# Performance work log

Measured on AMD Instinct MI355X. Metric: run time of the kernel, lower is better.

## Reference

```python
import jax, jax.numpy as jnp
import numpy as np

HID, NH = 2048, 16
QLR, KVLR = 1536, 512
DR, DN, DQK, DV = 64, 128, 192, 128
S = 2048
EPS = 1e-06


def rmsnorm(x, w, eps=EPS):
    return x * jax.lax.rsqrt(jnp.mean(x * x, axis=-1, keepdims=True) + eps) * w


def rope_interleave(x, cos, sin):
    # x: [B,H,S,D]; cos/sin: [B,S,D] (unsqueezed to head dim 1)
    b, h, s, d = x.shape
    # DeepSeek-V3 interleave: (d//2, 2) -> transpose -> flatten
    x = x.reshape(b, h, s, d // 2, 2).swapaxes(3, 4).reshape(b, h, s, d)
    c = cos[:, None, :, :]
    sn = sin[:, None, :, :]
    x1, x2 = x[..., : d // 2], x[..., d // 2:]
    rot = jnp.concatenate([-x2, x1], axis=-1)
    return x * c + rot * sn


def setup_inputs() -> dict:
    key = jax.random.key(0)
    ks = jax.random.split(key, 8)
    hidden_states = jax.random.normal(ks[0], (1, S, HID), dtype=jnp.float32)
    # real RoPE tables for the 64-dim rope part
    inv_freq = 1.0 / (10000.0 ** (np.arange(0, DR, 2, dtype=np.float32) / DR))
    pos = np.arange(S, dtype=np.float32)
    freqs = pos[:, None] * inv_freq[None, :]          # [S, DR/2]
    emb = np.concatenate([freqs, freqs], axis=-1)     # [S, DR]
    cos = jnp.asarray(np.cos(emb), dtype=jnp.float32)[None]
    sin = jnp.asarray(np.sin(emb), dtype=jnp.float32)[None]
    w = 0.02
    wq_a = jax.random.normal(ks[1], (QLR, HID), dtype=jnp.float32) * w
    q_a_ln_w = jnp.ones((QLR,), dtype=jnp.float32)
    wq_b = jax.random.normal(ks[2], (NH * DQK, QLR), dtype=jnp.float32) * w
    wkv_a = jax.random.normal(ks[3], (KVLR + DR, HID), dtype=jnp.float32) * w
    kv_a_ln_w = jnp.ones((KVLR,), dtype=jnp.float32)
    wkv_b = jax.random.normal(ks[4], (NH * (DN + DV), KVLR), dtype=jnp.float32) * w
    wo = jax.random.normal(ks[5], (HID, NH * DV), dtype=jnp.float32) * w
    cu_seqlens = jnp.array([0, S // 2, S], dtype=jnp.int32)  # two packed docs
    return {"hidden_states": hidden_states, "cos": cos, "sin": sin,
            "wq_a": wq_a, "q_a_ln_w": q_a_ln_w, "wq_b": wq_b,
            "wkv_a": wkv_a, "kv_a_ln_w": kv_a_ln_w, "wkv_b": wkv_b,
            "wo": wo, "cu_seqlens": cu_seqlens, "max_seqlen": S // 2}


def reference(hidden_states, cos, sin, wq_a, q_a_ln_w, wq_b, wkv_a, kv_a_ln_w,
              wkv_b, wo, cu_seqlens, max_seqlen):
    B, s, _ = hidden_states.shape
    # LoRA-compressed Q: q_a -> RMSNorm -> q_b
    q = rmsnorm(hidden_states @ wq_a.T, q_a_ln_w) @ wq_b.T       # [B,S,NH*DQK]
    q = q.reshape(B, s, NH, DQK).transpose(0, 2, 1, 3)           # [B,NH,S,DQK]
    q_pass, q_rot = q[..., :DN], q[..., DN:]
    # compressed KV with MQA rope part
    ckv = hidden_states @ wkv_a.T                                 # [B,S,KVLR+DR]
    kv_c, k_rot = ckv[..., :KVLR], ckv[..., KVLR:]
    kv = rmsnorm(kv_c, kv_a_ln_w) @ wkv_b.T                       # [B,S,NH*(DN+DV)]
    kv = kv.reshape(B, s, NH, DN + DV).transpose(0, 2, 1, 3)      # [B,NH,S,DN+DV]
    k_pass, v = kv[..., :DN], kv[..., DN:]
    k_rot = k_rot[:, None, :, :]                                  # [B,1,S,DR]
    q_rot = rope_interleave(q_rot, cos, sin)
    k_rot = rope_interleave(k_rot, cos, sin)
    k_rot = jnp.broadcast_to(k_rot, (B, NH, s, DR))
    qf = jnp.concatenate([q_pass, q_rot], axis=-1)                # [B,NH,S,DQK]
    kf = jnp.concatenate([k_pass, k_rot], axis=-1)                # [B,NH,S,DQK]
    # varlen causal attention: block-diagonal per document + causal
    pos = jnp.arange(s)
    seg = jnp.searchsorted(cu_seqlens[1:], pos, side='right')
    mask = (seg[:, None] == seg[None, :]) & (pos[:, None] >= pos[None, :])
    scale = DQK ** -0.5  # flash default: 1/sqrt(q head dim) (v padded to DQK)
    scores = jnp.einsum('bhqd,bhkd->bhqk', qf, kf) * scale
    scores = jnp.where(mask[None, None], scores, jnp.finfo(scores.dtype).min)
    attn = jax.nn.softmax(scores, axis=-1)
    out = jnp.einsum('bhqk,bhkd->bhqd', attn, v)                  # [B,NH,S,DV]
    out = out.transpose(0, 2, 1, 3).reshape(B, s, NH * DV)
    return out @ wo.T
```

## Files before the change

### kernel.cpp

```cpp
#include <hip/hip_runtime.h>

typedef unsigned short u16;
typedef __attribute__((ext_vector_type(8))) short bf16x8;
typedef __attribute__((ext_vector_type(4))) float f32x4;

#define HID 2048
#define NH 16
#define QLR 1536
#define KVLR 512
#define DR 64
#define DN 128
#define DQK 192
#define DV 128
#define SEQ 2048
#define NKVA 2176
#define SCALE 0.07216878364870323f
#define SCL2 0.1041164359699839f
#define THR2 11.541560327111707f

static __device__ __forceinline__ u16 f2bf(float f) {
  unsigned v = __builtin_bit_cast(unsigned, f);
  v = v + 0x7fffu + ((v >> 16) & 1u);
  return (u16)(v >> 16);
}
static __device__ __forceinline__ float bf2f(u16 u) {
  unsigned v = ((unsigned)u) << 16;
  return __builtin_bit_cast(float, v);
}

#define GLOAD16(gp, lp)                                                        \
  __builtin_amdgcn_global_load_lds(                                            \
      (const __attribute__((address_space(1))) void*)(gp),                     \
      (__attribute__((address_space(3))) void*)(lp), 16, 0, 0)

__global__ void k_convert_all(const float* __restrict__ hs, const float* __restrict__ wq_a,
                              const float* __restrict__ wkv_a, const float* __restrict__ wqb,
                              const float* __restrict__ wkvb, const float* __restrict__ wo,
                              u16* __restrict__ hs_bf, u16* __restrict__ wqkva,
                              u16* __restrict__ wqb_bf, u16* __restrict__ wkvb_bf,
                              u16* __restrict__ wo_bf) {
  const long NQ = 4915200;
  long q = (long)blockIdx.x * blockDim.x + threadIdx.x;
  const long stride = (long)gridDim.x * blockDim.x;
  for (; q < NQ; q += stride) {
    const float* src;
    u16* dst;
    long li;
    bool zero = false;
    if (q < 1048576)        { src = hs;   dst = hs_bf;                      li = q; }
    else if (q < 1835008)   { src = wq_a; dst = wqkva;                      li = q - 1048576; }
    else if (q < 2162688)   { li = q - 1835008; src = wkv_a; dst = wqkva + (size_t)QLR * HID;
                              zero = (li >= 294912); }
    else if (q < 3342336)   { src = wqb;  dst = wqb_bf;                     li = q - 2162688; }
    else if (q < 3866624)   { src = wkvb; dst = wkvb_bf;                    li = q - 3342336; }
    else                    { src = wo;   dst = wo_bf;                      li = q - 3866624; }
    u16 o0 = 0, o1 = 0, o2 = 0, o3 = 0;
    if (!zero) {
      const float4 f = *(const float4*)(src + li * 4);
      o0 = f2bf(f.x); o1 = f2bf(f.y); o2 = f2bf(f.z); o3 = f2bf(f.w);
    }
    u16* d = dst + li * 4;
    d[0] = o0; d[1] = o1; d[2] = o2; d[3] = o3;
  }
}

__global__ void k_rmsnorm2(const float* __restrict__ qkva, const float* __restrict__ qw,
                           const float* __restrict__ kvw, u16* __restrict__ q_ln,
                           u16* __restrict__ kv_ln) {
  const int row = blockIdx.x;
  const int which = blockIdx.y;
  const int t = threadIdx.x;
  const int cols = which ? KVLR : QLR;
  const float inv_cols = which ? (1.0f / KVLR) : (1.0f / QLR);
  const float* x = qkva + (size_t)row * NKVA + (which ? QLR : 0);
  const float* w = which ? kvw : qw;
  u16* Y = (which ? kv_ln : q_ln) + (size_t)row * cols;
  float ss = 0.f;
  for (int i = t * 4; i < cols; i += 1024) {
    float4 v = *(const float4*)(x + i);
    ss += v.x * v.x + v.y * v.y + v.z * v.z + v.w * v.w;
  }
#pragma unroll
  for (int m = 1; m < 64; m <<= 1) ss += __shfl_xor(ss, m, 64);
  __shared__ float red[4];
  if ((t & 63) == 0) red[t >> 6] = ss;
  __syncthreads();
  float tot = red[0] + red[1] + red[2] + red[3];
  float r = rsqrtf(tot * inv_cols + 1e-6f);
  for (int i = t * 4; i < cols; i += 1024) {
    float4 v = *(const float4*)(x + i);
    float4 g = *(const float4*)(w + i);
    u16* y = Y + i;
    y[0] = f2bf(v.x * r * g.x);
    y[1] = f2bf(v.y * r * g.y);
    y[2] = f2bf(v.z * r * g.z);
    y[3] = f2bf(v.w * r * g.w);
  }
}

template <int WN, int NBUF, int MODE>
__global__ __launch_bounds__(512) void k_gemm_nt8(
    const u16* __restrict__ A, const u16* __restrict__ B, void* __restrict__ Cout,
    int M, int N, int K, const float* __restrict__ cosb, const float* __restrict__ sinb,
    u16* __restrict__ out_a, u16* __restrict__ out_b) {
  constexpr int BN = WN * 64;
  constexpr int NST = 2 + WN;
  __shared__ __align__(16) u16 As[NBUF][128 * 64];
  __shared__ __align__(16) u16 Bs[NBUF][BN * 64];
  __shared__ __align__(16) u16 vts[MODE == 3 ? 128 * 130 : 2];
  const int t = threadIdx.x;
  const int lane = t & 63;
  const int w = t >> 6, wr = w >> 2, wc = w & 3;
  const int lm = lane & 15, lg = lane >> 4;

  const int nwg = gridDim.x * gridDim.y;
  int bid = blockIdx.y * gridDim.x + blockIdx.x;
  if ((nwg & 7) == 0) bid = (bid & 7) * (nwg >> 3) + (bid >> 3);
  const int bm = bid % gridDim.y;
  const int bn = bid / gridDim.y;

  const u16* aT = A + (size_t)bm * 128 * K;
  const u16* bT = B + (size_t)bn * BN * K;

#define STAGE8(buf, kt_)                                                       \
  do {                                                                         \
    _Pragma("unroll") for (int i = 0; i < 2; ++i) {                            \
      const int g = t + i * 512, row = g >> 3, slot = (g & 7) ^ (row & 7);     \
      GLOAD16(aT + (size_t)row * K + slot * 8 + (kt_), (u16*)As[buf] + g * 8); \
    }                                                                          \
    _Pragma("unroll") for (int i = 0; i < WN; ++i) {                           \
      const int g = t + i * 512, row = g >> 3, slot = (g & 7) ^ (row & 7);     \
      GLOAD16(bT + (size_t)row * K + slot * 8 + (kt_), (u16*)Bs[buf] + g * 8); \
    }                                                                          \
  } while (0)

  f32x4 acc[4][WN] = {};
  const int nk = K >> 6;
#pragma unroll
  for (int b = 0; b < NBUF; ++b)
    if (b < nk) STAGE8(b, b << 6);
  int bt = 0;
  for (int kt = 0; kt < nk; ++kt) {
    const int rem = nk - 1 - kt;
    if constexpr (NBUF == 3) {
      if (rem >= 2)      asm volatile("s_waitcnt vmcnt(%0)" :: "i"(2 * NST) : "memory");
      else if (rem == 1) asm volatile("s_waitcnt vmcnt(%0)" :: "i"(NST) : "memory");
      else               asm volatile("s_waitcnt vmcnt(0)" ::: "memory");
    } else {
      if (rem >= 1)      asm volatile("s_waitcnt vmcnt(%0)" :: "i"(NST) : "memory");
      else               asm volatile("s_waitcnt vmcnt(0)" ::: "memory");
    }
    __builtin_amdgcn_s_barrier();
    __builtin_amdgcn_sched_barrier(0);
    bf16x8 af[2][4], bfr[2][WN];
#pragma unroll
    for (int kk = 0; kk < 2; ++kk) {
#pragma unroll
      for (int i = 0; i < 4; ++i) {
        const int row_ = wr * 64 + i * 16 + lm;
        af[kk][i] = *(const bf16x8*)(As[bt] + row_ * 64 +
                                     ((((kk << 2) | lg) ^ (row_ & 7)) << 3));
      }
#pragma unroll
      for (int j = 0; j < WN; ++j) {
        const int row_ = wc * (WN * 16) + j * 16 + lm;
        bfr[kk][j] = *(const bf16x8*)(Bs[bt] + row_ * 64 +
                                      ((((kk << 2) | lg) ^ (row_ & 7)) << 3));
      }
    }
    asm volatile("s_waitcnt lgkmcnt(0)" ::: "memory");
    __builtin_amdgcn_sched_barrier(0);
    __builtin_amdgcn_s_barrier();
    __builtin_amdgcn_sched_barrier(0);
    if (kt + NBUF < nk) STAGE8(bt, (kt + NBUF) << 6);
    __builtin_amdgcn_s_setprio(1);
#pragma unroll
    for (int kk = 0; kk < 2; ++kk)
#pragma unroll
      for (int i = 0; i < 4; ++i)
#pragma unroll
        for (int j = 0; j < WN; ++j)
          acc[i][j] = __builtin_amdgcn_mfma_f32_16x16x32_bf16(af[kk][i], bfr[kk][j],
                                                              acc[i][j], 0, 0, 0);
    __builtin_amdgcn_s_setprio(0);
    bt = (bt == NBUF - 1) ? 0 : bt + 1;
  }
#undef STAGE8

  const int row0 = bm * 128 + wr * 64 + lg * 4;
  const int col0 = bn * BN + wc * (WN * 16) + lm;
  if constexpr (MODE == 1) {
    u16* C = (u16*)Cout;
#pragma unroll
    for (int i = 0; i < 4; ++i)
#pragma unroll
      for (int r = 0; r < 4; ++r) {
        u16* crow = C + (size_t)(row0 + i * 16 + r) * N + col0;
#pragma unroll
        for (int j = 0; j < WN; ++j) crow[j * 16] = f2bf(acc[i][j][r]);
      }
  } else if constexpr (MODE == 0) {
    float* C = (float*)Cout;
#pragma unroll
    for (int i = 0; i < 4; ++i)
#pragma unroll
      for (int r = 0; r < 4; ++r) {
        float* crow = C + (size_t)(row0 + i * 16 + r) * N + col0;
#pragma unroll
        for (int j = 0; j < WN; ++j) crow[j * 16] = acc[i][j][r];
      }
  } else if constexpr (MODE == 2) {
    const int h = bn;
#pragma unroll
    for (int i = 0; i < 4; ++i)
#pragma unroll
      for (int r = 0; r < 4; ++r) {
        const int s = row0 + i * 16 + r;
        u16* qrow = out_a + ((size_t)h * SEQ + s) * DQK;
#pragma unroll
        for (int j = 0; j < WN; ++j) {
          const int c = wc * 48 + j * 16 + lm;
          float val = acc[i][j][r];
          float partner = __shfl_xor(val, 1, 64);
          if (c < 128) {
            qrow[c] = f2bf(val * SCL2);
          } else {
            const int u = c - 128, p = u >> 1, od = u & 1;
            float cv = cosb[(size_t)s * DR + p];
            float sv = sinb[(size_t)s * DR + p];
            float o = od ? (val * cv + partner * sv) : (val * cv - partner * sv);
            qrow[128 + od * 32 + p] = f2bf(o * SCL2);
          }
        }
      }
  } else {
    const int h = bn;
    const int sl0 = wr * 64 + lg * 4;
#pragma unroll
    for (int i = 0; i < 4; ++i)
#pragma unroll
      for (int r = 0; r < 4; ++r) {
        const int s = row0 + i * 16 + r;
        const int sl = sl0 + i * 16 + r;
#pragma unroll
        for (int j = 0; j < WN; ++j) {
          const int c = wc * 64 + j * 16 + lm;
          const u16 bv = f2bf(acc[i][j][r]);
          if (c < 128) out_a[((size_t)h * SEQ + s) * DQK + c] = bv;
          else vts[(c - 128) * 130 + sl] = bv;
        }
      }
    __syncthreads();
    const int d = t >> 2, q4 = t & 3;
#pragma unroll
    for (int sub = 0; sub < 4; ++sub) {
      bf16x8 v;
#pragma unroll
      for (int e = 0; e < 8; ++e) v[e] = (short)vts[d * 130 + q4 * 32 + sub * 8 + e];
      *(bf16x8*)(out_b + ((size_t)h * DV + d) * SEQ + bm * 128 + q4 * 32 + sub * 8) = v;
    }
  }
}

__global__ __launch_bounds__(256) void k_rope_k(
    const float* __restrict__ krot, int stride, const float* __restrict__ cosb,
    const float* __restrict__ sinb, u16* __restrict__ kf) {
  const int s0 = blockIdx.x * 32;
  const int t = threadIdx.x;
  const int row = t >> 3, c8 = t & 7;
  const int s = s0 + row;
  const int half = c8 >> 2, p0 = (c8 & 3) * 8;
  bf16x8 v;
#pragma unroll
  for (int e = 0; e < 8; ++e) {
    const int p = p0 + e;
    float a = krot[(size_t)s * stride + 2 * p];
    float b = krot[(size_t)s * stride + 2 * p + 1];
    float cv = cosb[(size_t)s * DR + p];
    float sv = sinb[(size_t)s * DR + p];
    v[e] = (short)f2bf(half ? (b * cv + a * sv) : (a * cv - b * sv));
  }
#pragma unroll
  for (int h = 0; h < NH; ++h)
    *(bf16x8*)(kf + ((size_t)h * SEQ + s) * DQK + 128 + half * 32 + p0) = v;
}

__global__ __launch_bounds__(256) void k_attn(
    const u16* __restrict__ qf, const u16* __restrict__ kf, const u16* __restrict__ vt,
    u16* __restrict__ attn_out, float* __restrict__ O_part, float* __restrict__ mlbuf) {
  __shared__ __align__(16) u16 Ks[2][32 * 192];
  __shared__ __align__(16) u16 Vs[2][128 * 32];
  __shared__ __align__(16) u16 p_lds[4][16][32];

  static const signed char TJ[24] = {15,15,7,14,14,13,13,6,12,12,11,11,5,
                                     10,10,9,9,4,8,8,3,2,1,0};
  static const signed char CK[24] = {0,1,2,0,1,0,1,2,0,1,0,1,2,
                                     0,1,0,1,2,0,1,2,2,2,2};

  const int t = threadIdx.x, lane = t & 63, w = t >> 6;
  const int lm = lane & 15, lg = lane >> 4;
  const int bid = blockIdx.x;
  const int x = bid & 7, rr = bid >> 3;
  const int hh = rr & 1, idx = rr >> 1;
  const int seg = idx & 1, slot = idx >> 1;
  const int tj = TJ[slot], ck = CK[slot];
  const int h = x * 2 + hh;
  const int tile_row0 = seg * 1024 + tj * 64;
  const int k_begin = seg * 1024;
  const int n_all = 2 * tj + 2;
  const int kt_lo = (ck == 1) ? (tj + 1) : 0;
  const int kt_hi = (ck == 0) ? (tj + 1) : n_all;
  const int n_kt = kt_hi - kt_lo;

  const int lo_row = tile_row0 + w * 16;
  bf16x8 qfr[6];
  {
    const u16* qp = qf + ((size_t)h * SEQ + (lo_row + lm)) * DQK + lg * 8;
#pragma unroll
    for (int c = 0; c < 6; ++c) qfr[c] = *(const bf16x8*)(qp + c * 32);
  }
  int qrow[4];
#pragma unroll
  for (int r = 0; r < 4; ++r) qrow[r] = lo_row + lg * 4 + r;

  float m_r[4], l_loc[4];
#pragma unroll
  for (int r = 0; r < 4; ++r) { m_r[r] = -3.0e4f; l_loc[r] = 0.f; }
  f32x4 oacc[8] = {};
  bf16x8 pa, vv[8];

#define STAGEA(buf, kt_)                                                       \
  do {                                                                         \
    const int k0_ = k_begin + (kt_) * 32;                                      \
    _Pragma("unroll") for (int p = 0; p < 3; ++p) {                            \
      const int id = p * 256 + t;                                              \
      const int row = id / 24, colL = id - row * 24;                           \
      const u16* g = kf + ((size_t)h * SEQ + k0_ + row) * DQK +                \
                     ((colL ^ (row & 7)) * 8);                                 \
      GLOAD16(g, (u16*)Ks[buf] + id * 8);                                      \
    }                                                                          \
    _Pragma("unroll") for (int p = 0; p < 2; ++p) {                            \
      const int id = p * 256 + t;                                              \
      const int row = id >> 2, colL = id & 3;                                  \
      const u16* g = vt + ((size_t)h * DV + row) * SEQ + k0_ +                 \
                     ((colL ^ (row & 3)) * 8);                                 \
      GLOAD16(g, (u16*)Vs[buf] + id * 8);                                      \
    }                                                                          \
  } while (0)

#define COMPUTE1(buf, kt_)                                                     \
  do {                                                                         \
    const int k0_ = k_begin + (kt_) * 32;                                      \
    f32x4 sc[2] = {};                                                          \
    __builtin_amdgcn_s_setprio(1);                                             \
    _Pragma("unroll") for (int n0_ = 0; n0_ < 2; ++n0_)                        \
        _Pragma("unroll") for (int c_ = 0; c_ < 6; ++c_) {                     \
      const int row_ = n0_ * 16 + lm, cc_ = c_ * 4 + lg;                       \
      bf16x8 kfr = *(const bf16x8*)(Ks[buf] + row_ * 192 +                     \
                                    ((cc_ ^ (row_ & 7)) * 8));                 \
      sc[n0_] = __builtin_amdgcn_mfma_f32_16x16x32_bf16(qfr[c_], kfr,          \
                                                        sc[n0_], 0, 0, 0);     \
    }                                                                          \
    __builtin_amdgcn_s_setprio(0);                                             \
    _Pragma("unroll") for (int nd = 0; nd < 8; ++nd) {                         \
      const int row_ = nd * 16 + lm;                                           \
      vv[nd] = *(const bf16x8*)(Vs[buf] + row_ * 32 +                          \
                                ((lg ^ (row_ & 3)) * 8));                      \
    }                                                                          \
    float s0a[4], s1a[4];                                                      \
    float over = -1e30f;                                                       \
    if (lo_row >= k0_ + 31) {                                                  \
      _Pragma("unroll") for (int r = 0; r < 4; ++r) {                          \
        s0a[r] = sc[0][r];                                                     \
        s1a[r] = sc[1][r];                                                     \
        over = fmaxf(over, fmaxf(s0a[r], s1a[r]) - m_r[r]);                    \
      }                                                                        \
    } else {                                                                   \
      const int kc0 = k0_ + lm, kc1 = k0_ + 16 + lm;                           \
      _Pragma("unroll") for (int r = 0; r < 4; ++r) {                          \
        s0a[r] = (kc0 <= qrow[r]) ? sc[0][r] : -1e30f;                         \
        s1a[r] = (kc1 <= qrow[r]) ? sc[1][r] : -1e30f;                         \
        over = fmaxf(over, fmaxf(s0a[r], s1a[r]) - m_r[r]);                    \
      }                                                                        \
    }                                                                          \
    if (__any(over > THR2)) {                                                  \
      _Pragma("unroll") for (int r = 0; r < 4; ++r) {                          \
        float mx = fmaxf(s0a[r], s1a[r]);                                      \
        _Pragma("unroll") for (int md = 1; md < 16; md <<= 1)                  \
            mx = fmaxf(mx, __shfl_xor(mx, md, 64));                            \
        float mnew = fmaxf(m_r[r], mx);                                        \
        float alpha = exp2f(m_r[r] - mnew);                                    \
        m_r[r] = mnew;                                                         \
        l_loc[r] *= alpha;                                                     \
        _Pragma("unroll") for (int nd = 0; nd < 8; ++nd) oacc[nd][r] *= alpha; \
      }                                                                        \
    }                                                                          \
    _Pragma("unroll") for (int r = 0; r < 4; ++r) {                            \
      float p0 = exp2f(s0a[r] - m_r[r]);                                       \
      float p1 = exp2f(s1a[r] - m_r[r]);                                       \
      l_loc[r] += p0 + p1;                                                     \
      p_lds[w][lg * 4 + r][lm] = f2bf(p0);                                     \
      p_lds[w][lg * 4 + r][16 + lm] = f2bf(p1);                                \
    }                                                                          \
    asm volatile("s_waitcnt lgkmcnt(0)" ::: "memory");                         \
    __builtin_amdgcn_sched_barrier(0);                                         \
    pa = *(const bf16x8*)(&p_lds[w][lm][lg * 8]);                              \
  } while (0)

  STAGEA(0, kt_lo);
  STAGEA(1, kt_lo + 1);
  for (int i = 0; i < n_kt; ++i) {
    const int kt = kt_lo + i;
    if (i + 1 < n_kt) asm volatile("s_waitcnt vmcnt(5)" ::: "memory");
    else              asm volatile("s_waitcnt vmcnt(0)" ::: "memory");
    __builtin_amdgcn_s_barrier();
    __builtin_amdgcn_sched_barrier(0);
    COMPUTE1(i & 1, kt);
    asm volatile("s_waitcnt lgkmcnt(0)" ::: "memory");
    __builtin_amdgcn_sched_barrier(0);
    __builtin_amdgcn_s_barrier();
    __builtin_amdgcn_sched_barrier(0);
    if (i + 2 < n_kt) STAGEA(i & 1, kt + 2);
    __builtin_amdgcn_s_setprio(1);
#pragma unroll
    for (int nd = 0; nd < 8; ++nd)
      oacc[nd] = __builtin_amdgcn_mfma_f32_16x16x32_bf16(pa, vv[nd], oacc[nd], 0, 0, 0);
    __builtin_amdgcn_s_setprio(0);
  }
#undef STAGEA
#undef COMPUTE1

  float l_row[4];
#pragma unroll
  for (int r = 0; r < 4; ++r) {
    float lt = l_loc[r];
#pragma unroll
    for (int md = 1; md < 16; md <<= 1) lt += __shfl_xor(lt, md, 64);
    l_row[r] = lt;
  }

  if (ck == 2) {
#pragma unroll
    for (int r = 0; r < 4; ++r) {
      float inv = 1.0f / l_row[r];
#pragma unroll
      for (int nd = 0; nd < 8; ++nd)
        attn_out[(size_t)qrow[r] * (NH * DV) + h * DV + nd * 16 + lm] =
            f2bf(oacc[nd][r] * inv);
    }
  } else {
    const int part = (((tj - 8) * 2 + seg) * 16 + h) * 2 + ck;
    float* op = O_part + (size_t)part * 8192;
#pragma unroll
    for (int r = 0; r < 4; ++r) {
      const int rw = w * 16 + lg * 4 + r;
#pragma unroll
      for (int nd = 0; nd < 8; ++nd)
        op[rw * 128 + nd * 16 + lm] = oacc[nd][r];
      if (lm == 0) {
        mlbuf[part * 128 + rw] = m_r[r];
        mlbuf[part * 128 + 64 + rw] = l_row[r];
      }
    }
  }
}

__global__ __launch_bounds__(256) void k_merge(const float* __restrict__ O_part,
                                               const float* __restrict__ mlbuf,
                                               u16* __restrict__ attn_out) {
  const int b = blockIdx.x;
  const int h = b & 15, z = b >> 4;
  const int tj = 8 + (z >> 1), seg = z & 1;
  const int p0 = (((tj - 8) * 2 + seg) * 16 + h) * 2;
  const int p1 = p0 + 1;
  const int t = threadIdx.x;
  const int row = t >> 2, cg = t & 3;

  const float m0 = mlbuf[p0 * 128 + row], l0 = mlbuf[p0 * 128 + 64 + row];
  const float m1 = mlbuf[p1 * 128 + row], l1 = mlbuf[p1 * 128 + 64 + row];
  const float M = fmaxf(m0, m1);
  const float w0 = exp2f(m0 - M), w1 = exp2f(m1 - M);
  const float inv = 1.0f / (w0 * l0 + w1 * l1);
  const float a0 = w0 * inv, a1 = w1 * inv;

  const int qrow = seg * 1024 + tj * 64 + row;
  const float* o0 = O_part + (size_t)p0 * 8192 + row * 128 + cg * 32;
  const float* o1 = O_part + (size_t)p1 * 8192 + row * 128 + cg * 32;
  u16* dst = attn_out + (size_t)qrow * (NH * DV) + h * DV + cg * 32;
#pragma unroll
  for (int e = 0; e < 32; e += 4) {
    const float4 u = *(const float4*)(o0 + e);
    const float4 v = *(const float4*)(o1 + e);
    dst[e]     = f2bf(a0 * u.x + a1 * v.x);
    dst[e + 1] = f2bf(a0 * u.y + a1 * v.y);
    dst[e + 2] = f2bf(a0 * u.z + a1 * v.z);
    dst[e + 3] = f2bf(a0 * u.w + a1 * v.w);
  }
}

extern "C" void kernel_launch(void* const* d_in, const int* in_sizes, int n_in,
                              void* d_out, int out_size, void* d_ws, size_t ws_size,
                              hipStream_t stream) {
  const float* hs = (const float*)d_in[0];
  const float* cosb = (const float*)d_in[1];
  const float* sinb = (const float*)d_in[2];
  const float* wq_a = (const float*)d_in[3];
  const float* q_a_ln_w = (const float*)d_in[4];
  const float* wq_b = (const float*)d_in[5];
  const float* wkv_a = (const float*)d_in[6];
  const float* kv_a_ln_w = (const float*)d_in[7];
  const float* wkv_b = (const float*)d_in[8];
  const float* wo = (const float*)d_in[9];

  char* ws = (char*)d_ws;
  size_t off = 0;
  auto take = [&](size_t bytes) {
    size_t o = off;
    off += (bytes + 255) & ~(size_t)255;
    return o;
  };
  u16* hs_bf = (u16*)(ws + take((size_t)SEQ * HID * 2));
  u16* wqkva = (u16*)(ws + take((size_t)NKVA * HID * 2));
  u16* wqb = (u16*)(ws + take((size_t)(NH * DQK) * QLR * 2));
  u16* wkvb = (u16*)(ws + take((size_t)(NH * 256) * KVLR * 2));
  u16* wo_bf = (u16*)(ws + take((size_t)HID * (NH * DV) * 2));
  float* qkva = (float*)(ws + take((size_t)SEQ * NKVA * 4));
  u16* q_ln = (u16*)(ws + take((size_t)SEQ * QLR * 2));
  u16* kv_ln = (u16*)(ws + take((size_t)SEQ * KVLR * 2));
  u16* qf = (u16*)(ws + take((size_t)NH * SEQ * DQK * 2));
  u16* kf = (u16*)(ws + take((size_t)NH * SEQ * DQK * 2));
  u16* vt = (u16*)(ws + take((size_t)NH * DV * SEQ * 2));
  u16* attn = (u16*)(ws + take((size_t)SEQ * NH * DV * 2));
  float* O_part = (float*)(ws + take((size_t)512 * 8192 * 4));
  float* mlbuf = (float*)(ws + take((size_t)512 * 128 * 4));
  if (off > ws_size) return;

  k_convert_all<<<2048, 256, 0, stream>>>(hs, wq_a, wkv_a, wq_b, wkv_b, wo,
                                          hs_bf, wqkva, wqb, wkvb, wo_bf);

  dim3 g1(NKVA / 128, SEQ / 128);
  k_gemm_nt8<2, 2, 0><<<g1, 512, 0, stream>>>(hs_bf, wqkva, qkva, SEQ, NKVA, HID,
                                              nullptr, nullptr, nullptr, nullptr);

  k_rmsnorm2<<<dim3(SEQ, 2), 256, 0, stream>>>(qkva, q_a_ln_w, kv_a_ln_w, q_ln, kv_ln);

  k_rope_k<<<SEQ / 32, 256, 0, stream>>>(qkva + (QLR + KVLR), NKVA, cosb, sinb, kf);

  dim3 g2(NH * DQK / 192, SEQ / 128);
  k_gemm_nt8<3, 2, 2><<<g2, 512, 0, stream>>>(q_ln, wqb, nullptr, SEQ, NH * DQK, QLR,
                                              cosb, sinb, qf, nullptr);
  dim3 g3(NH * 256 / 256, SEQ / 128);
  k_gemm_nt8<4, 2, 3><<<g3, 512, 0, stream>>>(kv_ln, wkvb, nullptr, SEQ, NH * 256, KVLR,
                                              nullptr, nullptr, kf, vt);

  k_attn<<<768, 256, 0, stream>>>(qf, kf, vt, attn, O_part, mlbuf);
  k_merge<<<256, 256, 0, stream>>>(O_part, mlbuf, attn);

  dim3 g4(HID / 128, SEQ / 128);
  k_gemm_nt8<2, 2, 0><<<g4, 512, 0, stream>>>(attn, wo_bf, d_out, SEQ, HID, NH * DV,
                                              nullptr, nullptr, nullptr, nullptr);
}
```

Measured before the change: 184.4 us.

## Stage 64-key K tiles in LDS, read V directly from global, rebalance split schedule

```diff
diff --git a/kernel.cpp b/kernel.cpp
--- a/kernel.cpp
+++ b/kernel.cpp
@@ -288,14 +288,13 @@
 __global__ __launch_bounds__(256) void k_attn(
     const u16* __restrict__ qf, const u16* __restrict__ kf, const u16* __restrict__ vt,
     u16* __restrict__ attn_out, float* __restrict__ O_part, float* __restrict__ mlbuf) {
-  __shared__ __align__(16) u16 Ks[2][32 * 192];
-  __shared__ __align__(16) u16 Vs[2][128 * 32];
+  __shared__ __align__(16) u16 Ks[2][64 * 192];
   __shared__ __align__(16) u16 p_lds[4][16][32];
 
-  static const signed char TJ[24] = {15,15,7,14,14,13,13,6,12,12,11,11,5,
-                                     10,10,9,9,4,8,8,3,2,1,0};
-  static const signed char CK[24] = {0,1,2,0,1,0,1,2,0,1,0,1,2,
-                                     0,1,0,1,2,0,1,2,2,2,2};
+  static const signed char TJ[24] = {15,15,14,7, 14,13,13,12,6, 12,11,11,10,5,
+                                     10,9,9,8,4, 8,3, 2, 1, 0};
+  static const signed char CK[24] = {0,1,0,2, 1,0,1,0,2, 1,0,1,0,2,
+                                     1,0,1,0,2, 1,2, 2, 2, 2};
 
   const int t = threadIdx.x, lane = t & 63, w = t >> 6;
   const int lm = lane & 15, lg = lane >> 4;
@@ -307,10 +306,10 @@
   const int h = x * 2 + hh;
   const int tile_row0 = seg * 1024 + tj * 64;
   const int k_begin = seg * 1024;
-  const int n_all = 2 * tj + 2;
-  const int kt_lo = (ck == 1) ? (tj + 1) : 0;
-  const int kt_hi = (ck == 0) ? (tj + 1) : n_all;
-  const int n_kt = kt_hi - kt_lo;
+  const int h0 = (tj + 2) >> 1;
+  const int u_lo = (ck == 1) ? h0 : 0;
+  const int u_hi = (ck == 0) ? h0 : (tj + 1);
+  const int nst = u_hi - u_lo;
 
   const int lo_row = tile_row0 + w * 16;
   bf16x8 qfr[6];
@@ -329,54 +328,45 @@
   f32x4 oacc[8] = {};
   bf16x8 pa, vv[8];
 
-#define STAGEA(buf, kt_)                                                       \
+#define STAGEA(buf, u_)                                                        \
   do {                                                                         \
-    const int k0_ = k_begin + (kt_) * 32;                                      \
-    _Pragma("unroll") for (int p = 0; p < 3; ++p) {                            \
+    const int k0_ = k_begin + (u_) * 64;                                       \
+    _Pragma("unroll") for (int p = 0; p < 6; ++p) {                            \
       const int id = p * 256 + t;                                              \
       const int row = id / 24, colL = id - row * 24;                           \
       const u16* g = kf + ((size_t)h * SEQ + k0_ + row) * DQK +                \
                      ((colL ^ (row & 7)) * 8);                                 \
       GLOAD16(g, (u16*)Ks[buf] + id * 8);                                      \
     }                                                                          \
-    _Pragma("unroll") for (int p = 0; p < 2; ++p) {                            \
-      const int id = p * 256 + t;                                              \
-      const int row = id >> 2, colL = id & 3;                                  \
-      const u16* g = vt + ((size_t)h * DV + row) * SEQ + k0_ +                 \
-                     ((colL ^ (row & 3)) * 8);                                 \
-      GLOAD16(g, (u16*)Vs[buf] + id * 8);                                      \
-    }                                                                          \
   } while (0)
 
-#define COMPUTE1(buf, kt_)                                                     \
+#define COMPUTE1(buf, sub, k0_)                                                \
   do {                                                                         \
-    const int k0_ = k_begin + (kt_) * 32;                                      \
     f32x4 sc[2] = {};                                                          \
     __builtin_amdgcn_s_setprio(1);                                             \
     _Pragma("unroll") for (int n0_ = 0; n0_ < 2; ++n0_)                        \
         _Pragma("unroll") for (int c_ = 0; c_ < 6; ++c_) {                     \
       const int row_ = n0_ * 16 + lm, cc_ = c_ * 4 + lg;                       \
-      bf16x8 kfr = *(const bf16x8*)(Ks[buf] + row_ * 192 +                     \
+      bf16x8 kfr = *(const bf16x8*)(Ks[buf] + ((sub) * 32 + row_) * 192 +      \
                                     ((cc_ ^ (row_ & 7)) * 8));                 \
       sc[n0_] = __builtin_amdgcn_mfma_f32_16x16x32_bf16(qfr[c_], kfr,          \
                                                         sc[n0_], 0, 0, 0);     \
     }                                                                          \
     __builtin_amdgcn_s_setprio(0);                                             \
     _Pragma("unroll") for (int nd = 0; nd < 8; ++nd) {                         \
-      const int row_ = nd * 16 + lm;                                           \
-      vv[nd] = *(const bf16x8*)(Vs[buf] + row_ * 32 +                          \
-                                ((lg ^ (row_ & 3)) * 8));                      \
+      vv[nd] = *(const bf16x8*)(vt + ((size_t)h * DV + nd * 16 + lm) * SEQ +   \
+                                (k0_) + lg * 8);                               \
     }                                                                          \
     float s0a[4], s1a[4];                                                      \
     float over = -1e30f;                                                       \
-    if (lo_row >= k0_ + 31) {                                                  \
+    if (lo_row >= (k0_) + 31) {                                                \
       _Pragma("unroll") for (int r = 0; r < 4; ++r) {                          \
         s0a[r] = sc[0][r];                                                     \
         s1a[r] = sc[1][r];                                                     \
         over = fmaxf(over, fmaxf(s0a[r], s1a[r]) - m_r[r]);                    \
       }                                                                        \
     } else {                                                                   \
-      const int kc0 = k0_ + lm, kc1 = k0_ + 16 + lm;                           \
+      const int kc0 = (k0_) + lm, kc1 = (k0_) + 16 + lm;                       \
       _Pragma("unroll") for (int r = 0; r < 4; ++r) {                          \
         s0a[r] = (kc0 <= qrow[r]) ? sc[0][r] : -1e30f;                         \
         s1a[r] = (kc1 <= qrow[r]) ? sc[1][r] : -1e30f;                         \
@@ -407,28 +397,38 @@
     pa = *(const bf16x8*)(&p_lds[w][lm][lg * 8]);                              \
   } while (0)
 
-  STAGEA(0, kt_lo);
-  STAGEA(1, kt_lo + 1);
-  for (int i = 0; i < n_kt; ++i) {
-    const int kt = kt_lo + i;
-    if (i + 1 < n_kt) asm volatile("s_waitcnt vmcnt(5)" ::: "memory");
-    else              asm volatile("s_waitcnt vmcnt(0)" ::: "memory");
+#define PVSTEP                                                                 \
+  do {                                                                         \
+    __builtin_amdgcn_s_setprio(1);                                             \
+    _Pragma("unroll") for (int nd = 0; nd < 8; ++nd)                           \
+        oacc[nd] =                                                             \
+        __builtin_amdgcn_mfma_f32_16x16x32_bf16(pa, vv[nd], oacc[nd], 0, 0, 0);\
+    __builtin_amdgcn_s_setprio(0);                                             \
+  } while (0)
+
+  STAGEA(0, u_lo);
+  if (nst > 1) STAGEA(1, u_lo + 1);
+  int bt = 0;
+  for (int i = 0; i < nst; ++i) {
+    const int u = u_lo + i;
+    if (i + 1 < nst) asm volatile("s_waitcnt vmcnt(6)" ::: "memory");
+    else             asm volatile("s_waitcnt vmcnt(0)" ::: "memory");
     __builtin_amdgcn_s_barrier();
     __builtin_amdgcn_sched_barrier(0);
-    COMPUTE1(i & 1, kt);
+    COMPUTE1(bt, 0, k_begin + u * 64);
+    PVSTEP;
+    COMPUTE1(bt, 1, k_begin + u * 64 + 32);
     asm volatile("s_waitcnt lgkmcnt(0)" ::: "memory");
     __builtin_amdgcn_sched_barrier(0);
     __builtin_amdgcn_s_barrier();
     __builtin_amdgcn_sched_barrier(0);
-    if (i + 2 < n_kt) STAGEA(i & 1, kt + 2);
-    __builtin_amdgcn_s_setprio(1);
-#pragma unroll
-    for (int nd = 0; nd < 8; ++nd)
-      oacc[nd] = __builtin_amdgcn_mfma_f32_16x16x32_bf16(pa, vv[nd], oacc[nd], 0, 0, 0);
-    __builtin_amdgcn_s_setprio(0);
+    if (i + 2 < nst) STAGEA(bt, u + 2);
+    PVSTEP;
+    bt ^= 1;
   }
 #undef STAGEA
 #undef COMPUTE1
+#undef PVSTEP
 
   float l_row[4];
 #pragma unroll
```

Measured after the change: 197.1 us. +6.9%, slower.
